# Kernel tuning notes

Measured on AMD Instinct MI355X. Metric: run time of the kernel, lower is better.

Reference implementation:

```python
import jax, jax.numpy as jnp
import numpy as np

D_MODEL = 1024
N_HEAD = 16
HEAD_DIM = D_MODEL // N_HEAD


def setup_inputs() -> dict:
    key = jax.random.key(0)
    k1, k2, k3 = jax.random.split(key, 3)
    B, T = 2, 2048
    x = jax.random.normal(k1, (B, T, D_MODEL), dtype=jnp.float32)
    # nn.MultiheadAttention packed in-projection: (3*D, D), xavier-like scale
    w_in = jax.random.normal(k2, (3 * D_MODEL, D_MODEL), dtype=jnp.float32) * (1.0 / np.sqrt(D_MODEL))
    b_in = jnp.zeros((3 * D_MODEL,), dtype=jnp.float32)
    w_out = jax.random.normal(k3, (D_MODEL, D_MODEL), dtype=jnp.float32) * (1.0 / np.sqrt(D_MODEL))
    b_out = jnp.zeros((D_MODEL,), dtype=jnp.float32)
    return {"x": x, "w_in": w_in, "b_in": b_in, "w_out": w_out, "b_out": b_out}


def reference(x, w_in, b_in, w_out, b_out):
    B, T, D = x.shape
    H, hd = N_HEAD, HEAD_DIM
    # packed QKV projection (torch Linear convention: y = x @ W.T + b)
    qkv = x @ w_in.T + b_in                      # [B, T, 3D]
    q, k, v = jnp.split(qkv, 3, axis=-1)
    # [B, H, T, hd]
    q = q.reshape(B, T, H, hd).transpose(0, 2, 1, 3)
    k = k.reshape(B, T, H, hd).transpose(0, 2, 1, 3)
    v = v.reshape(B, T, H, hd).transpose(0, 2, 1, 3)
    scale = 1.0 / np.sqrt(hd).astype(np.float32)
    scores = jnp.einsum("bhqd,bhkd->bhqk", q * scale, k)  # [B, H, T, T]
    causal = jnp.tril(jnp.ones((T, T), dtype=bool))
    scores = jnp.where(causal, scores, jnp.finfo(scores.dtype).min)
    attn = jax.nn.softmax(scores, axis=-1)
    ctx = jnp.einsum("bhqk,bhkd->bhqd", attn, v)           # [B, H, T, hd]
    ctx = ctx.transpose(0, 2, 1, 3).reshape(B, T, D)
    return ctx @ w_out.T + b_out
```

## Files before the change

### kernel.cpp

```cpp
#include <hip/hip_runtime.h>


#define T_SEQ 2048
#define D_MODEL 1024
#define NEG_BIG (-1.0e30f)
#define Q_SCALE 0.18033688f

typedef float f32x4 __attribute__((ext_vector_type(4)));
typedef short s16x8 __attribute__((ext_vector_type(8)));
typedef __bf16 bf16x8 __attribute__((ext_vector_type(8)));

__device__ __forceinline__ f32x4 mfma16(s16x8 a, s16x8 b, f32x4 c) {
    return __builtin_amdgcn_mfma_f32_16x16x32_bf16(
        __builtin_bit_cast(bf16x8, a), __builtin_bit_cast(bf16x8, b), c, 0, 0, 0);
}

__device__ __forceinline__ short f2bf(float f) {
    unsigned int u = __float_as_uint(f);
    u += 0x7fffu + ((u >> 16) & 1u);
    return (short)(u >> 16);
}
__device__ __forceinline__ unsigned f2bfu(float f) {
    unsigned int u = __float_as_uint(f);
    u += 0x7fffu + ((u >> 16) & 1u);
    return u >> 16;
}
__device__ __forceinline__ unsigned f2bfu_fast(float f) {
    return (__float_as_uint(f) + 0x8000u) >> 16;
}
__device__ __forceinline__ float bf2f(short s) {
    return __uint_as_float(((unsigned int)(unsigned short)s) << 16);
}

__device__ __forceinline__ void async_lds16(const short* g, short* l) {
    __builtin_amdgcn_global_load_lds(
        (const __attribute__((address_space(1))) unsigned int*)g,
        (__attribute__((address_space(3))) unsigned int*)l, 16, 0, 0);
}

#define N_X   4194304
#define N_WI  3145728
#define N_BI  3072
#define N_WO  1048576
#define N_BO  1024
#define V_X   (N_X  / 4)
#define V_WI  (N_WI / 4)
#define V_BI  (N_BI / 4)
#define V_WO  (N_WO / 4)
#define V_BO  (N_BO / 4)
#define V_TOT (V_X + V_WI + V_BI + V_WO + V_BO)

__global__ __launch_bounds__(256) void canon_all_kernel(
    const float* __restrict__ x, const float* __restrict__ wi,
    const float* __restrict__ bi, const float* __restrict__ wo,
    const float* __restrict__ bo,
    short* __restrict__ xb, short* __restrict__ wib, short* __restrict__ bib,
    short* __restrict__ wob, short* __restrict__ bob)
{
    int i = blockIdx.x * 256 + threadIdx.x;
    if (i >= V_TOT) return;
    const float* src; short* dst; int off;
    if      (i < V_X)                    { src = x;  dst = xb;  off = i; }
    else if (i < V_X+V_WI)               { src = wi; dst = wib; off = i - V_X; }
    else if (i < V_X+V_WI+V_BI)          { src = bi; dst = bib; off = i - V_X - V_WI; }
    else if (i < V_X+V_WI+V_BI+V_WO)     { src = wo; dst = wob; off = i - V_X - V_WI - V_BI; }
    else                                 { src = bo; dst = bob; off = i - V_X - V_WI - V_BI - V_WO; }
    float4 v = ((const float4*)src)[off];
    short4 o = { f2bf(v.x), f2bf(v.y), f2bf(v.z), f2bf(v.w) };
    ((short4*)dst)[off] = o;
}

__global__ __launch_bounds__(256) void gemm_qkv_kernel(
    const short* __restrict__ A, const short* __restrict__ B,
    const short* __restrict__ bias,
    short* __restrict__ qo, short* __restrict__ ko, short* __restrict__ vt)
{
    const int K = 1024;
    alignas(16) __shared__ short As[128][32];
    alignas(16) __shared__ short Bs[128][32];
    const int m0 = blockIdx.x * 128;
    const int n0 = blockIdx.y * 128;
    const int tid = threadIdx.x;
    const int lane = tid & 63;
    const int w = tid >> 6;
    const int wm = (w >> 1) * 64, wn = (w & 1) * 64;
    const int quad = lane >> 4, l16 = lane & 15;

    f32x4 acc[4][4];
    const f32x4 zero = {0.f, 0.f, 0.f, 0.f};
#pragma unroll
    for (int i = 0; i < 4; ++i)
#pragma unroll
        for (int j = 0; j < 4; ++j) acc[i][j] = zero;

    const int lrow = lane >> 2;
    const int lcol = (lane & 3) * 8;
    const short* gA0 = &A[(m0 + w*32      + lrow) * K + lcol];
    const short* gA1 = &A[(m0 + w*32 + 16 + lrow) * K + lcol];
    const short* gB0 = &B[(n0 + w*32      + lrow) * K + lcol];
    const short* gB1 = &B[(n0 + w*32 + 16 + lrow) * K + lcol];
    short* lA0 = &As[w*32][0];
    short* lA1 = &As[w*32 + 16][0];
    short* lB0 = &Bs[w*32][0];
    short* lB1 = &Bs[w*32 + 16][0];

    for (int k0 = 0; k0 < K; k0 += 32) {
        __syncthreads();
        async_lds16(gA0 + k0, lA0);
        async_lds16(gA1 + k0, lA1);
        async_lds16(gB0 + k0, lB0);
        async_lds16(gB1 + k0, lB1);
        __syncthreads();

        s16x8 af[4], bfr[4];
#pragma unroll
        for (int i = 0; i < 4; ++i) af[i]  = *(const s16x8*)&As[wm + i*16 + l16][quad*8];
#pragma unroll
        for (int j = 0; j < 4; ++j) bfr[j] = *(const s16x8*)&Bs[wn + j*16 + l16][quad*8];
#pragma unroll
        for (int i = 0; i < 4; ++i)
#pragma unroll
            for (int j = 0; j < 4; ++j)
                acc[i][j] = mfma16(af[i], bfr[j], acc[i][j]);
    }

#pragma unroll
    for (int j = 0; j < 4; ++j) {
        int n = n0 + wn + j*16 + l16;
        float bi = bf2f(bias[n]);
        int which = n >> 10;
        int h = (n >> 6) & 15, d = n & 63;
        if (which == 2) {
#pragma unroll
            for (int i = 0; i < 4; ++i) {
                int tb = m0 + wm + i*16 + quad*4;
                int b = tb >> 11, t = tb & 2047;
                uint2 pk;
                pk.x = f2bfu(acc[i][j][0] + bi) | (f2bfu(acc[i][j][1] + bi) << 16);
                pk.y = f2bfu(acc[i][j][2] + bi) | (f2bfu(acc[i][j][3] + bi) << 16);
                *(uint2*)&vt[(((size_t)(b*16 + h)) * 64 + d) * 2048 + t] = pk;
            }
        } else {
            short* dst = (which == 0) ? qo : ko;
            float scl = (which == 0) ? Q_SCALE : 1.0f;
#pragma unroll
            for (int i = 0; i < 4; ++i) {
#pragma unroll
                for (int r = 0; r < 4; ++r) {
                    int m = m0 + wm + i*16 + quad*4 + r;
                    int b = m >> 11, t = m & 2047;
                    float v = (acc[i][j][r] + bi) * scl;
                    dst[(((b*16 + h) * 2048) + t) * 64 + d] = f2bf(v);
                }
            }
        }
    }
}

__global__ __launch_bounds__(256) void attn_kernel(
    const short* __restrict__ Q, const short* __restrict__ K,
    const short* __restrict__ Vt, short* __restrict__ ctx)
{
    alignas(16) __shared__ short Ks[64][72];
    alignas(16) __shared__ short Vs[64][72];
    alignas(16) __shared__ short Pl[4][16][72];

    const int bh = blockIdx.x;
    const int qt = 31 - (int)blockIdx.y;
    const int qbase = qt * 64;
    const int tid = threadIdx.x;
    const int w = tid >> 6, lane = tid & 63;
    const int quad = lane >> 4, l16 = lane & 15;
    const int b = bh >> 4, h = bh & 15;

    const short* Qb  = Q  + bh * T_SEQ * 64;
    const short* Kb  = K  + bh * T_SEQ * 64;
    const short* Vbt = Vt + bh * 64 * T_SEQ;

    const short* qrow = Qb + (qbase + w*16 + l16) * 64;
    const s16x8 qa0 = *(const s16x8*)(qrow + quad*8);
    const s16x8 qa1 = *(const s16x8*)(qrow + 32 + quad*8);

    const f32x4 zero = {0.f, 0.f, 0.f, 0.f};
    f32x4 o[4];
#pragma unroll
    for (int dt = 0; dt < 4; ++dt) o[dt] = zero;
    float lsum = 0.f;

    const int sr  = tid >> 3;
    const int scl = (tid & 7) * 8;
    const int qg  = qbase + w*16 + l16;

    for (int s0 = 0; s0 <= qbase; s0 += 64) {
        __syncthreads();
        *(float4*)&Ks[sr][scl]    = *(const float4*)&Kb[(s0 + sr) * 64 + scl];
        *(float4*)&Ks[sr+32][scl] = *(const float4*)&Kb[(s0 + sr + 32) * 64 + scl];
        *(float4*)&Vs[sr][scl]    = *(const float4*)&Vbt[(size_t)sr * T_SEQ + s0 + scl];
        *(float4*)&Vs[sr+32][scl] = *(const float4*)&Vbt[(size_t)(sr + 32) * T_SEQ + s0 + scl];
        __syncthreads();

#pragma unroll
        for (int sub = 0; sub < 4; ++sub) {
            s16x8 ka0 = *(const s16x8*)&Ks[sub*16 + l16][quad*8];
            s16x8 ka1 = *(const s16x8*)&Ks[sub*16 + l16][32 + quad*8];
            f32x4 S = mfma16(ka1, qa1, mfma16(ka0, qa0, zero));
            if (s0 == qbase) {
                int sb = s0 + sub*16 + quad*4;
#pragma unroll
                for (int r = 0; r < 4; ++r)
                    if (sb + r > qg) S[r] = NEG_BIG;
            }
            float p0 = exp2f(S[0]), p1 = exp2f(S[1]);
            float p2 = exp2f(S[2]), p3 = exp2f(S[3]);
            lsum += (p0 + p1) + (p2 + p3);
            uint2 pk;
            pk.x = f2bfu_fast(p0) | (f2bfu_fast(p1) << 16);
            pk.y = f2bfu_fast(p2) | (f2bfu_fast(p3) << 16);
            *(uint2*)&Pl[w][l16][sub*16 + quad*4] = pk;
        }

        s16x8 pb0 = *(const s16x8*)&Pl[w][l16][quad*8];
        s16x8 pb1 = *(const s16x8*)&Pl[w][l16][32 + quad*8];
#pragma unroll
        for (int dt = 0; dt < 4; ++dt) {
            s16x8 va0 = *(const s16x8*)&Vs[dt*16 + l16][quad*8];
            s16x8 va1 = *(const s16x8*)&Vs[dt*16 + l16][32 + quad*8];
            o[dt] = mfma16(va1, pb1, mfma16(va0, pb0, o[dt]));
        }
    }

    lsum += __shfl_xor(lsum, 16, 64);
    lsum += __shfl_xor(lsum, 32, 64);
    float inv = 1.0f / lsum;
    int base = (b * T_SEQ + qg) * D_MODEL + h * 64;
#pragma unroll
    for (int dt = 0; dt < 4; ++dt) {
        uint2 pk;
        pk.x = f2bfu(o[dt][0] * inv) | (f2bfu(o[dt][1] * inv) << 16);
        pk.y = f2bfu(o[dt][2] * inv) | (f2bfu(o[dt][3] * inv) << 16);
        *(uint2*)&ctx[base + dt*16 + quad*4] = pk;
    }
}

__global__ __launch_bounds__(256) void gemm_out_kernel(
    const short* __restrict__ A, const short* __restrict__ B,
    const short* __restrict__ bias, float* __restrict__ out)
{
    const int K = 1024;
    alignas(16) __shared__ short As[128][32];
    alignas(16) __shared__ short Bs[64][32];
    const int m0 = blockIdx.x * 128;
    const int n0 = blockIdx.y * 64;
    const int tid = threadIdx.x;
    const int lane = tid & 63;
    const int w = tid >> 6;
    const int wm = (w >> 1) * 64, wn = (w & 1) * 32;
    const int quad = lane >> 4, l16 = lane & 15;

    f32x4 acc[4][2];
    const f32x4 zero = {0.f, 0.f, 0.f, 0.f};
#pragma unroll
    for (int i = 0; i < 4; ++i)
#pragma unroll
        for (int j = 0; j < 2; ++j) acc[i][j] = zero;

    const int lrow = lane >> 2;
    const int lcol = (lane & 3) * 8;
    const short* gA0 = &A[(m0 + w*32      + lrow) * K + lcol];
    const short* gA1 = &A[(m0 + w*32 + 16 + lrow) * K + lcol];
    const short* gB0 = &B[(n0 + w*16      + lrow) * K + lcol];
    short* lA0 = &As[w*32][0];
    short* lA1 = &As[w*32 + 16][0];
    short* lB0 = &Bs[w*16][0];

    for (int k0 = 0; k0 < K; k0 += 32) {
        __syncthreads();
        async_lds16(gA0 + k0, lA0);
        async_lds16(gA1 + k0, lA1);
        async_lds16(gB0 + k0, lB0);
        __syncthreads();

        s16x8 af[4], bfr[2];
#pragma unroll
        for (int i = 0; i < 4; ++i) af[i]  = *(const s16x8*)&As[wm + i*16 + l16][quad*8];
#pragma unroll
        for (int j = 0; j < 2; ++j) bfr[j] = *(const s16x8*)&Bs[wn + j*16 + l16][quad*8];
#pragma unroll
        for (int i = 0; i < 4; ++i)
#pragma unroll
            for (int j = 0; j < 2; ++j)
                acc[i][j] = mfma16(af[i], bfr[j], acc[i][j]);
    }

#pragma unroll
    for (int j = 0; j < 2; ++j) {
        int n = n0 + wn + j*16 + l16;
        float bi = bf2f(bias[n]);
#pragma unroll
        for (int i = 0; i < 4; ++i) {
#pragma unroll
            for (int r = 0; r < 4; ++r) {
                int m = m0 + wm + i*16 + quad*4 + r;
                out[m * 1024 + n] = acc[i][j][r] + bi;
            }
        }
    }
}

extern "C" void kernel_launch(void* const* d_in, const int* in_sizes, int n_in,
                              void* d_out, int out_size, void* d_ws, size_t ws_size,
                              hipStream_t stream) {
    float* out = (float*)d_out;
    char* ws = (char*)d_ws;

    const size_t MB = 1u << 20;
    short* xb     = (short*)(ws);
    short* w_inb  = (short*)(ws + 8*MB);
    short* b_inb  = (short*)(ws + 14*MB);
    short* w_outb = (short*)(ws + 15*MB);
    short* b_outb = (short*)(ws + 17*MB);
    short* qb     = (short*)(ws + 18*MB);
    short* kb     = (short*)(ws + 26*MB);
    short* vtb    = (short*)(ws + 34*MB);
    short* ctxb   = (short*)(ws + 42*MB);

    canon_all_kernel<<<(V_TOT + 255) / 256, 256, 0, stream>>>(
        (const float*)d_in[0], (const float*)d_in[1], (const float*)d_in[2],
        (const float*)d_in[3], (const float*)d_in[4],
        xb, w_inb, b_inb, w_outb, b_outb);

    gemm_qkv_kernel<<<dim3(32, 24), 256, 0, stream>>>(xb, w_inb, b_inb, qb, kb, vtb);
    attn_kernel<<<dim3(32, 32), 256, 0, stream>>>(qb, kb, vtb, ctxb);
    gemm_out_kernel<<<dim3(32, 16), 256, 0, stream>>>(ctxb, w_outb, b_outb, out);
}
```

Baseline: 195.8 us.

## Deepen GEMM K-tiles, prefetch attention K/V into registers, add separate V transpose

Both GEMMs now stage 64-wide K slices per iteration instead of 32, which halves the number of barrier pairs and doubles the MFMA work done between them. The attention kernel loads the next K/V tile into registers while the current tile is being computed, so global load latency overlaps with compute. The QKV GEMM now writes V row-major like Q and K, and a new kernel transposes it into the reused xb buffer. This replaces the strided transposed stores but adds a launch and an extra pass over V.

```diff
diff --git a/kernel.cpp b/kernel.cpp
--- a/kernel.cpp
+++ b/kernel.cpp
@@ -73,11 +73,11 @@
 __global__ __launch_bounds__(256) void gemm_qkv_kernel(
     const short* __restrict__ A, const short* __restrict__ B,
     const short* __restrict__ bias,
-    short* __restrict__ qo, short* __restrict__ ko, short* __restrict__ vt)
+    short* __restrict__ qo, short* __restrict__ ko, short* __restrict__ vo)
 {
     const int K = 1024;
-    alignas(16) __shared__ short As[128][32];
-    alignas(16) __shared__ short Bs[128][32];
+    alignas(16) __shared__ short As[128][64];
+    alignas(16) __shared__ short Bs[128][64];
     const int m0 = blockIdx.x * 128;
     const int n0 = blockIdx.y * 128;
     const int tid = threadIdx.x;
@@ -93,35 +93,42 @@
 #pragma unroll
         for (int j = 0; j < 4; ++j) acc[i][j] = zero;
 
-    const int lrow = lane >> 2;
-    const int lcol = (lane & 3) * 8;
-    const short* gA0 = &A[(m0 + w*32      + lrow) * K + lcol];
-    const short* gA1 = &A[(m0 + w*32 + 16 + lrow) * K + lcol];
-    const short* gB0 = &B[(n0 + w*32      + lrow) * K + lcol];
-    const short* gB1 = &B[(n0 + w*32 + 16 + lrow) * K + lcol];
-    short* lA0 = &As[w*32][0];
-    short* lA1 = &As[w*32 + 16][0];
-    short* lB0 = &Bs[w*32][0];
-    short* lB1 = &Bs[w*32 + 16][0];
-
-    for (int k0 = 0; k0 < K; k0 += 32) {
-        __syncthreads();
-        async_lds16(gA0 + k0, lA0);
-        async_lds16(gA1 + k0, lA1);
-        async_lds16(gB0 + k0, lB0);
-        async_lds16(gB1 + k0, lB1);
-        __syncthreads();
-
-        s16x8 af[4], bfr[4];
-#pragma unroll
-        for (int i = 0; i < 4; ++i) af[i]  = *(const s16x8*)&As[wm + i*16 + l16][quad*8];
-#pragma unroll
-        for (int j = 0; j < 4; ++j) bfr[j] = *(const s16x8*)&Bs[wn + j*16 + l16][quad*8];
-#pragma unroll
-        for (int i = 0; i < 4; ++i)
-#pragma unroll
-            for (int j = 0; j < 4; ++j)
-                acc[i][j] = mfma16(af[i], bfr[j], acc[i][j]);
+    const int lr8 = lane >> 3;
+    const int lc8 = (lane & 7) * 8;
+    const short* gA[4]; const short* gB[4];
+    short* lA[4]; short* lB[4];
+#pragma unroll
+    for (int i = 0; i < 4; ++i) {
+        gA[i] = &A[(m0 + w*32 + i*8 + lr8) * K + lc8];
+        gB[i] = &B[(n0 + w*32 + i*8 + lr8) * K + lc8];
+        lA[i] = &As[w*32 + i*8][0];
+        lB[i] = &Bs[w*32 + i*8][0];
+    }
+
+    for (int k0 = 0; k0 < K; k0 += 64) {
+        __syncthreads();
+#pragma unroll
+        for (int i = 0; i < 4; ++i) {
+            async_lds16(gA[i] + k0, lA[i]);
+            async_lds16(gB[i] + k0, lB[i]);
+        }
+        __syncthreads();
+
+        s16x8 af[4][2], bfr[4][2];
+#pragma unroll
+        for (int i = 0; i < 4; ++i) {
+            af[i][0]  = *(const s16x8*)&As[wm + i*16 + l16][quad*8];
+            af[i][1]  = *(const s16x8*)&As[wm + i*16 + l16][32 + quad*8];
+            bfr[i][0] = *(const s16x8*)&Bs[wn + i*16 + l16][quad*8];
+            bfr[i][1] = *(const s16x8*)&Bs[wn + i*16 + l16][32 + quad*8];
+        }
+#pragma unroll
+        for (int h = 0; h < 2; ++h)
+#pragma unroll
+            for (int i = 0; i < 4; ++i)
+#pragma unroll
+                for (int j = 0; j < 4; ++j)
+                    acc[i][j] = mfma16(af[i][h], bfr[j][h], acc[i][j]);
     }
 
 #pragma unroll
@@ -129,32 +136,46 @@
         int n = n0 + wn + j*16 + l16;
         float bi = bf2f(bias[n]);
         int which = n >> 10;
+        short* dst = (which == 0) ? qo : (which == 1) ? ko : vo;
+        float scl = (which == 0) ? Q_SCALE : 1.0f;
         int h = (n >> 6) & 15, d = n & 63;
-        if (which == 2) {
-#pragma unroll
-            for (int i = 0; i < 4; ++i) {
-                int tb = m0 + wm + i*16 + quad*4;
-                int b = tb >> 11, t = tb & 2047;
-                uint2 pk;
-                pk.x = f2bfu(acc[i][j][0] + bi) | (f2bfu(acc[i][j][1] + bi) << 16);
-                pk.y = f2bfu(acc[i][j][2] + bi) | (f2bfu(acc[i][j][3] + bi) << 16);
-                *(uint2*)&vt[(((size_t)(b*16 + h)) * 64 + d) * 2048 + t] = pk;
+#pragma unroll
+        for (int i = 0; i < 4; ++i) {
+#pragma unroll
+            for (int r = 0; r < 4; ++r) {
+                int m = m0 + wm + i*16 + quad*4 + r;
+                int b = m >> 11, t = m & 2047;
+                float v = (acc[i][j][r] + bi) * scl;
+                dst[(((b*16 + h) * 2048) + t) * 64 + d] = f2bf(v);
             }
-        } else {
-            short* dst = (which == 0) ? qo : ko;
-            float scl = (which == 0) ? Q_SCALE : 1.0f;
-#pragma unroll
-            for (int i = 0; i < 4; ++i) {
-#pragma unroll
-                for (int r = 0; r < 4; ++r) {
-                    int m = m0 + wm + i*16 + quad*4 + r;
-                    int b = m >> 11, t = m & 2047;
-                    float v = (acc[i][j][r] + bi) * scl;
-                    dst[(((b*16 + h) * 2048) + t) * 64 + d] = f2bf(v);
-                }
-            }
-        }
-    }
+        }
+    }
+}
+
+__global__ __launch_bounds__(256) void transpose_v_kernel(
+    const short* __restrict__ V, short* __restrict__ Vt)
+{
+    alignas(16) __shared__ short buf[64][72];
+    const int bh = blockIdx.x;
+    const int t0 = blockIdx.y * 64;
+    const int tid = threadIdx.x;
+    const int r = tid >> 2;
+    const int c = (tid & 3) * 16;
+
+    const short* src = V + ((size_t)bh * T_SEQ + t0) * 64;
+    *(float4*)&buf[r][c]     = *(const float4*)&src[r * 64 + c];
+    *(float4*)&buf[r][c + 8] = *(const float4*)&src[r * 64 + c + 8];
+    __syncthreads();
+
+    s16x8 o0, o1;
+#pragma unroll
+    for (int k2 = 0; k2 < 8; ++k2) {
+        o0[k2] = buf[c + k2][r];
+        o1[k2] = buf[c + 8 + k2][r];
+    }
+    short* dst = Vt + ((size_t)bh * 64 + r) * T_SEQ + t0;
+    *(s16x8*)&dst[c]     = o0;
+    *(s16x8*)&dst[c + 8] = o1;
 }
 
 __global__ __launch_bounds__(256) void attn_kernel(
@@ -175,7 +196,7 @@
 
     const short* Qb  = Q  + bh * T_SEQ * 64;
     const short* Kb  = K  + bh * T_SEQ * 64;
-    const short* Vbt = Vt + bh * 64 * T_SEQ;
+    const short* Vbt = Vt + (size_t)bh * 64 * T_SEQ;
 
     const short* qrow = Qb + (qbase + w*16 + l16) * 64;
     const s16x8 qa0 = *(const s16x8*)(qrow + quad*8);
@@ -191,13 +212,25 @@
     const int scl = (tid & 7) * 8;
     const int qg  = qbase + w*16 + l16;
 
+    float4 kf0 = *(const float4*)&Kb[sr * 64 + scl];
+    float4 kf1 = *(const float4*)&Kb[(sr + 32) * 64 + scl];
+    float4 vf0 = *(const float4*)&Vbt[(size_t)sr * T_SEQ + scl];
+    float4 vf1 = *(const float4*)&Vbt[(size_t)(sr + 32) * T_SEQ + scl];
+
     for (int s0 = 0; s0 <= qbase; s0 += 64) {
         __syncthreads();
-        *(float4*)&Ks[sr][scl]    = *(const float4*)&Kb[(s0 + sr) * 64 + scl];
-        *(float4*)&Ks[sr+32][scl] = *(const float4*)&Kb[(s0 + sr + 32) * 64 + scl];
-        *(float4*)&Vs[sr][scl]    = *(const float4*)&Vbt[(size_t)sr * T_SEQ + s0 + scl];
-        *(float4*)&Vs[sr+32][scl] = *(const float4*)&Vbt[(size_t)(sr + 32) * T_SEQ + s0 + scl];
-        __syncthreads();
+        *(float4*)&Ks[sr][scl]    = kf0;
+        *(float4*)&Ks[sr+32][scl] = kf1;
+        *(float4*)&Vs[sr][scl]    = vf0;
+        *(float4*)&Vs[sr+32][scl] = vf1;
+        __syncthreads();
+
+        if (s0 + 64 <= qbase) {
+            kf0 = *(const float4*)&Kb[(s0 + 64 + sr) * 64 + scl];
+            kf1 = *(const float4*)&Kb[(s0 + 64 + sr + 32) * 64 + scl];
+            vf0 = *(const float4*)&Vbt[(size_t)sr * T_SEQ + s0 + 64 + scl];
+            vf1 = *(const float4*)&Vbt[(size_t)(sr + 32) * T_SEQ + s0 + 64 + scl];
+        }
 
 #pragma unroll
         for (int sub = 0; sub < 4; ++sub) {
@@ -247,8 +280,8 @@
     const short* __restrict__ bias, float* __restrict__ out)
 {
     const int K = 1024;
-    alignas(16) __shared__ short As[128][32];
-    alignas(16) __shared__ short Bs[64][32];
+    alignas(16) __shared__ short As[128][64];
+    alignas(16) __shared__ short Bs[64][64];
     const int m0 = blockIdx.x * 128;
     const int n0 = blockIdx.y * 64;
     const int tid = threadIdx.x;
@@ -264,32 +297,45 @@
 #pragma unroll
         for (int j = 0; j < 2; ++j) acc[i][j] = zero;
 
-    const int lrow = lane >> 2;
-    const int lcol = (lane & 3) * 8;
-    const short* gA0 = &A[(m0 + w*32      + lrow) * K + lcol];
-    const short* gA1 = &A[(m0 + w*32 + 16 + lrow) * K + lcol];
-    const short* gB0 = &B[(n0 + w*16      + lrow) * K + lcol];
-    short* lA0 = &As[w*32][0];
-    short* lA1 = &As[w*32 + 16][0];
+    const int lr8 = lane >> 3;
+    const int lc8 = (lane & 7) * 8;
+    const short* gA[4]; short* lA[4];
+#pragma unroll
+    for (int i = 0; i < 4; ++i) {
+        gA[i] = &A[(m0 + w*32 + i*8 + lr8) * K + lc8];
+        lA[i] = &As[w*32 + i*8][0];
+    }
+    const short* gB0 = &B[(n0 + w*16 + lr8) * K + lc8];
+    const short* gB1 = &B[(n0 + w*16 + 8 + lr8) * K + lc8];
     short* lB0 = &Bs[w*16][0];
-
-    for (int k0 = 0; k0 < K; k0 += 32) {
-        __syncthreads();
-        async_lds16(gA0 + k0, lA0);
-        async_lds16(gA1 + k0, lA1);
+    short* lB1 = &Bs[w*16 + 8][0];
+
+    for (int k0 = 0; k0 < K; k0 += 64) {
+        __syncthreads();
+#pragma unroll
+        for (int i = 0; i < 4; ++i) async_lds16(gA[i] + k0, lA[i]);
         async_lds16(gB0 + k0, lB0);
-        __syncthreads();
-
-        s16x8 af[4], bfr[2];
-#pragma unroll
-        for (int i = 0; i < 4; ++i) af[i]  = *(const s16x8*)&As[wm + i*16 + l16][quad*8];
-#pragma unroll
-        for (int j = 0; j < 2; ++j) bfr[j] = *(const s16x8*)&Bs[wn + j*16 + l16][quad*8];
-#pragma unroll
-        for (int i = 0; i < 4; ++i)
-#pragma unroll
-            for (int j = 0; j < 2; ++j)
-                acc[i][j] = mfma16(af[i], bfr[j], acc[i][j]);
+        async_lds16(gB1 + k0, lB1);
+        __syncthreads();
+
+        s16x8 af[4][2], bfr[2][2];
+#pragma unroll
+        for (int i = 0; i < 4; ++i) {
+            af[i][0] = *(const s16x8*)&As[wm + i*16 + l16][quad*8];
+            af[i][1] = *(const s16x8*)&As[wm + i*16 + l16][32 + quad*8];
+        }
+#pragma unroll
+        for (int j = 0; j < 2; ++j) {
+            bfr[j][0] = *(const s16x8*)&Bs[wn + j*16 + l16][quad*8];
+            bfr[j][1] = *(const s16x8*)&Bs[wn + j*16 + l16][32 + quad*8];
+        }
+#pragma unroll
+        for (int h = 0; h < 2; ++h)
+#pragma unroll
+            for (int i = 0; i < 4; ++i)
+#pragma unroll
+                for (int j = 0; j < 2; ++j)
+                    acc[i][j] = mfma16(af[i][h], bfr[j][h], acc[i][j]);
     }
 
 #pragma unroll
@@ -321,15 +367,17 @@
     short* b_outb = (short*)(ws + 17*MB);
     short* qb     = (short*)(ws + 18*MB);
     short* kb     = (short*)(ws + 26*MB);
-    short* vtb    = (short*)(ws + 34*MB);
+    short* vb     = (short*)(ws + 34*MB);
     short* ctxb   = (short*)(ws + 42*MB);
+    short* vtb    = xb;
 
     canon_all_kernel<<<(V_TOT + 255) / 256, 256, 0, stream>>>(
         (const float*)d_in[0], (const float*)d_in[1], (const float*)d_in[2],
         (const float*)d_in[3], (const float*)d_in[4],
         xb, w_inb, b_inb, w_outb, b_outb);
 
-    gemm_qkv_kernel<<<dim3(32, 24), 256, 0, stream>>>(xb, w_inb, b_inb, qb, kb, vtb);
+    gemm_qkv_kernel<<<dim3(32, 24), 256, 0, stream>>>(xb, w_inb, b_inb, qb, kb, vb);
+    transpose_v_kernel<<<dim3(32, 32), 256, 0, stream>>>(vb, vtb);
     attn_kernel<<<dim3(32, 32), 256, 0, stream>>>(qb, kb, vtb, ctxb);
     gemm_out_kernel<<<dim3(32, 16), 256, 0, stream>>>(ctxb, w_outb, b_outb, out);
 }
```

Measured after the change: 194.8 us. Within noise of the previous version (-0.5%).
